# Kernel tuning notes

Hardware: AMD Instinct MI355X
Metric: run time of the kernel (lower is better)

Reference implementation:

```python
import jax, jax.numpy as jnp
import numpy as np

NEG = -1.0e4          # finite stand-in for log(0) to keep grads nan-free
DEN_SCALE = 1.0
B, T, P = 32, 500, 2048
S_DEN, S_NUM = 1024, 128


def setup_inputs() -> dict:
    key = jax.random.key(0)
    k0, k1 = jax.random.split(key)
    x = jax.random.normal(k0, (B, T, P), dtype=jnp.float32)
    seqlengths = jax.random.randint(k1, (B,), T // 2, T + 1)

    rng = np.random.default_rng(0)
    # --- denominator FSM (shared phone-LM lattice): self-loop + banded + random arcs ---
    idx = np.arange(S_DEN)
    mask = np.zeros((S_DEN, S_DEN), bool)
    for off in (0, 1, 2, 5):
        mask[idx, (idx + off) % S_DEN] = True
    mask[idx, rng.integers(0, S_DEN, S_DEN)] = True  # long-range arcs
    logw = rng.normal(0.0, 0.5, (S_DEN, S_DEN)).astype(np.float32)
    den_logT = jnp.asarray(np.where(mask, logw, NEG).astype(np.float32))
    den_init = jnp.full((S_DEN,), -np.log(S_DEN), dtype=jnp.float32)
    den_final = jnp.zeros((S_DEN,), dtype=jnp.float32)
    den_pdfmap = jnp.asarray(rng.integers(0, P, S_DEN))

    # --- numerator FSMs (per-utterance left-to-right alignment graphs) ---
    j = np.arange(S_NUM)
    nmask = np.zeros((S_NUM, S_NUM), bool)
    nmask[j, j] = True               # self-loops
    nmask[j[:-1], j[:-1] + 1] = True  # forward arcs
    nlogw = rng.normal(0.0, 0.5, (B, S_NUM, S_NUM)).astype(np.float32)
    num_logT = jnp.asarray(np.where(nmask[None], nlogw, NEG).astype(np.float32))
    num_init = jnp.asarray(np.where(j == 0, 0.0, NEG).astype(np.float32))
    nf = np.full(S_NUM, NEG, np.float32); nf[-1] = 0.0
    num_final = jnp.asarray(nf)
    num_pdfmap = jnp.asarray(rng.integers(0, P, (B, S_NUM)))

    return {
        'input': x, 'seqlengths': seqlengths,
        'den_logT': den_logT, 'den_init': den_init, 'den_final': den_final,
        'den_pdfmap': den_pdfmap,
        'num_logT': num_logT, 'num_init': num_init, 'num_final': num_final,
        'num_pdfmap': num_pdfmap,
    }


def _fsm_logmarginal(emis, seqlengths, logT, init, final):
    """Forward (alpha) recursion; returns per-utterance log-marginal [B].

    emis: [B,T,S] state emission log-likelihoods (already pdf-mapped)
    logT: [S,S] shared or [B,S,S] per-utterance log transition weights
    """
    Tmat = jnp.exp(logT)  # NEG -> ~0, recovers the sparse arc structure
    Bx, Tlen, S = emis.shape
    alpha = jnp.broadcast_to(init, (Bx, S)) + emis[:, 0]  # [B,S]

    def step(alpha, xt):
        e_t, t = xt
        # numerically stable log-matmul: logsumexp_i(alpha_i + logT_ij)
        m = jnp.max(alpha, axis=1, keepdims=True)            # [B,1]
        p = jnp.exp(alpha - m)                               # [B,S]
        if Tmat.ndim == 2:
            s = p @ Tmat                                     # [B,S]
        else:
            s = jnp.einsum('bi,bij->bj', p, Tmat)
        new = e_t + m + jnp.log(jnp.maximum(s, 1e-30))
        return jnp.where(t < seqlengths[:, None], new, alpha), None

    xs = (jnp.swapaxes(emis[:, 1:], 0, 1), jnp.arange(1, Tlen))
    alpha, _ = jax.lax.scan(step, alpha, xs)
    return jax.nn.logsumexp(alpha + final, axis=1)  # [B]


def reference(input, seqlengths, den_logT, den_init, den_final, den_pdfmap,
              num_logT, num_init, num_final, num_pdfmap):
    # map state -> pdf emission scores
    num_emis = jnp.take_along_axis(input, num_pdfmap[:, None, :], axis=2)  # [B,T,S_NUM]
    den_emis = input[:, :, den_pdfmap]                                      # [B,T,S_DEN]
    num_llh = jnp.sum(_fsm_logmarginal(num_emis, seqlengths, num_logT, num_init, num_final))
    den_llh = jnp.sum(_fsm_logmarginal(den_emis, seqlengths, den_logT, den_init, den_final))
    return -(num_llh - DEN_SCALE * den_llh)
```

## Files before the change

kernel.cpp:

```cpp
#include <hip/hip_runtime.h>

namespace {

constexpr int B = 32, T = 500, P = 2048;
constexpr int SD = 1024, SN = 128;
constexpr float NZ_THRESH = -5000.0f;
constexpr int MAXE = 12;

#define BAR_LDS() asm volatile("s_waitcnt lgkmcnt(0)\n\ts_barrier" ::: "memory")

template<int CTRL>
__device__ __forceinline__ float dpp_mov(float v, float old) {
  return __builtin_bit_cast(float, __builtin_amdgcn_update_dpp(
      __builtin_bit_cast(int, old), __builtin_bit_cast(int, v),
      CTRL, 0xf, 0xf, false));
}

__device__ __forceinline__ float wave_max_bcast(float v) {
  v = fmaxf(v, dpp_mov<0x111>(v, v));
  v = fmaxf(v, dpp_mov<0x112>(v, v));
  v = fmaxf(v, dpp_mov<0x114>(v, v));
  v = fmaxf(v, dpp_mov<0x118>(v, v));
  v = fmaxf(v, dpp_mov<0x142>(v, v));
  v = fmaxf(v, dpp_mov<0x143>(v, v));
  return __builtin_bit_cast(float,
      __builtin_amdgcn_readlane(__builtin_bit_cast(int, v), 63));
}

__device__ __forceinline__ float wave_sum_bcast(float v) {
  v += dpp_mov<0x111>(v, 0.0f);
  v += dpp_mov<0x112>(v, 0.0f);
  v += dpp_mov<0x114>(v, 0.0f);
  v += dpp_mov<0x118>(v, 0.0f);
  v += dpp_mov<0x142>(v, 0.0f);
  v += dpp_mov<0x143>(v, 0.0f);
  return __builtin_bit_cast(float,
      __builtin_amdgcn_readlane(__builtin_bit_cast(int, v), 63));
}

__device__ __forceinline__ float max4(float a, float b, float c, float d) {
  return fmaxf(fmaxf(a, b), fmaxf(c, d));
}


__global__ void k_init(int* __restrict__ rcount, float* __restrict__ out) {
  int i = blockIdx.x * blockDim.x + threadIdx.x;
  if (i < SD) rcount[i] = 0;
  if (i == 0) out[0] = 0.0f;
}

__device__ __forceinline__ bool is_det(int i, int j) {
  int off = (j - i) & (SD - 1);
  return off == 0 || off == 1 || off == 2 || off == 5;
}

__global__ void k_count(const float* __restrict__ dlogT, int* __restrict__ rcount) {
  int idx = blockIdx.x * blockDim.x + threadIdx.x;
  if (idx >= SD * SD) return;
  int i = idx >> 10, j = idx & (SD - 1);
  float v = dlogT[idx];
  if (v > NZ_THRESH && !is_det(i, j)) atomicAdd(&rcount[j], 1);
}

__global__ __launch_bounds__(1024) void k_scan(const int* __restrict__ rcount,
                                               int* __restrict__ rptr,
                                               int* __restrict__ wpos) {
  __shared__ int sA[SD], sB[SD];
  int tid = threadIdx.x;
  int v = rcount[tid];
  sA[tid] = v;
  __syncthreads();
  int* src = sA; int* dst = sB;
  for (int off = 1; off < SD; off <<= 1) {
    int val = src[tid];
    if (tid >= off) val += src[tid - off];
    dst[tid] = val;
    __syncthreads();
    int* t = src; src = dst; dst = t;
  }
  int inc = src[tid];
  rptr[tid + 1] = inc;
  if (tid == 0) rptr[0] = 0;
  wpos[tid] = inc - v;
}

__global__ void k_fill(const float* __restrict__ dlogT, int* __restrict__ wpos,
                       int2* __restrict__ compact) {
  int idx = blockIdx.x * blockDim.x + threadIdx.x;
  if (idx >= SD * SD) return;
  int i = idx >> 10, j = idx & (SD - 1);
  float v = dlogT[idx];
  if (v > NZ_THRESH && !is_det(i, j)) {
    int pos = atomicAdd(&wpos[j], 1);
    if (pos < 1024) compact[pos] = make_int2(i, __float_as_int(__expf(v)));
  }
}


__global__ __launch_bounds__(256) void lfmmi_main(
    const float* __restrict__ x, const int* __restrict__ seqlen,
    const float* __restrict__ dlogT, const float* __restrict__ dinit,
    const float* __restrict__ dfinal, const int* __restrict__ dpdf,
    const float* __restrict__ nlogT, const float* __restrict__ ninit,
    const float* __restrict__ nfinal, const int* __restrict__ npdf,
    const int* __restrict__ rptr, const int2* __restrict__ redge,
    float* __restrict__ out) {
  int bid = blockIdx.x;
  int tid = threadIdx.x;

  if (bid < B) {
    __shared__ __align__(16) float lp[SD + 8];
    __shared__ __align__(16) float wred[4];
    __shared__ int2 sedge[1024];

    const int b = bid;
    int L = seqlen[b]; if (L > T) L = T; if (L < 1) L = 1;
    const int s0 = tid * 4;
    const float* xb = x + (long)b * T * P;

    int nnz = rptr[SD]; if (nnz > 1024) nnz = 1024;
    for (int k = tid; k < nnz; k += 256) sedge[k] = redge[k];

    float dw[4][4];
    const int offs[4] = {0, 1, 2, 5};
#pragma unroll
    for (int i = 0; i < 4; ++i) {
      int j = s0 + i;
#pragma unroll
      for (int o = 0; o < 4; ++o) {
        int r = (j - offs[o]) & (SD - 1);
        dw[i][o] = __expf(dlogT[r * SD + j]);
      }
    }

    const int pdf0 = dpdf[s0], pdf1 = dpdf[s0 + 1], pdf2 = dpdf[s0 + 2], pdf3 = dpdf[s0 + 3];
    const int r0 = rptr[s0], r1 = rptr[s0 + 1], r2 = rptr[s0 + 2],
              r3 = rptr[s0 + 3], r4 = rptr[s0 + 4];

    int   erow[MAXE];
    float ew0[MAXE], ew1[MAXE], ew2[MAXE], ew3[MAXE];
#pragma unroll
    for (int s = 0; s < MAXE; ++s) {
      int k = r0 + s;
      bool valid = k < r4;
      int kk = valid ? k : 0;
      int2 e = redge[kk];
      erow[s] = valid ? e.x : 0;
      float w = __int_as_float(e.y);
      ew0[s] = (valid && k <  r1) ? w : 0.0f;
      ew1[s] = (valid && k >= r1 && k < r2) ? w : 0.0f;
      ew2[s] = (valid && k >= r2 && k < r3) ? w : 0.0f;
      ew3[s] = (valid && k >= r3) ? w : 0.0f;
    }
    const bool overflow = (r4 - r0) > MAXE;

    float4 al;
    al.x = dinit[s0]     + xb[pdf0];
    al.y = dinit[s0 + 1] + xb[pdf1];
    al.z = dinit[s0 + 2] + xb[pdf2];
    al.w = dinit[s0 + 3] + xb[pdf3];

    float4 ec, en, ef;
    ec.x = xb[P + pdf0];     ec.y = xb[P + pdf1];     ec.z = xb[P + pdf2];     ec.w = xb[P + pdf3];
    en.x = xb[2 * P + pdf0]; en.y = xb[2 * P + pdf1]; en.z = xb[2 * P + pdf2]; en.w = xb[2 * P + pdf3];

    __syncthreads();

    for (int t = 1; t < L; ++t) {
      float mw = wave_max_bcast(max4(al.x, al.y, al.z, al.w));
      if ((tid & 63) == 0) wred[tid >> 6] = mw;
      BAR_LDS();
      float4 wv = *(const float4*)wred;
      float m = max4(wv.x, wv.y, wv.z, wv.w);

      float4 p;
      p.x = expf(al.x - m); p.y = expf(al.y - m);
      p.z = expf(al.z - m); p.w = expf(al.w - m);
      *(float4*)&lp[8 + s0] = p;
      if (tid >= 254) *(float4*)&lp[8 + s0 - SD] = p;

      {
        int tp = t + 2; if (tp > T - 1) tp = T - 1;
        const float* xr = xb + tp * P;
        ef.x = xr[pdf0]; ef.y = xr[pdf1]; ef.z = xr[pdf2]; ef.w = xr[pdf3];
      }
      BAR_LDS();

      float4 w = *(const float4*)&lp[8 + s0 - 4];
      float pm5 = lp[8 + s0 - 5];
      float acc0 = p.x * dw[0][0] + w.w * dw[0][1] + w.z * dw[0][2] + pm5 * dw[0][3];
      float acc1 = p.y * dw[1][0] + p.x * dw[1][1] + w.w * dw[1][2] + w.x * dw[1][3];
      float acc2 = p.z * dw[2][0] + p.y * dw[2][1] + p.x * dw[2][2] + w.y * dw[2][3];
      float acc3 = p.w * dw[3][0] + p.z * dw[3][1] + p.y * dw[3][2] + w.z * dw[3][3];

#pragma unroll
      for (int s = 0; s < MAXE; ++s) {
        float val = lp[8 + erow[s]];
        acc0 += val * ew0[s];
        acc1 += val * ew1[s];
        acc2 += val * ew2[s];
        acc3 += val * ew3[s];
      }
      if (overflow) {
        for (int k = r0 + MAXE; k < r4; ++k) {
          int2 e = sedge[k];
          float val = lp[8 + e.x] * __int_as_float(e.y);
          if (k < r1) acc0 += val; else if (k < r2) acc1 += val;
          else if (k < r3) acc2 += val; else acc3 += val;
        }
      }

      al.x = ec.x + m + logf(fmaxf(acc0, 1e-30f));
      al.y = ec.y + m + logf(fmaxf(acc1, 1e-30f));
      al.z = ec.z + m + logf(fmaxf(acc2, 1e-30f));
      al.w = ec.w + m + logf(fmaxf(acc3, 1e-30f));
      ec = en; en = ef;
    }

    float4 v;
    v.x = al.x + dfinal[s0];     v.y = al.y + dfinal[s0 + 1];
    v.z = al.z + dfinal[s0 + 2]; v.w = al.w + dfinal[s0 + 3];
    float mw = wave_max_bcast(max4(v.x, v.y, v.z, v.w));
    if ((tid & 63) == 0) wred[tid >> 6] = mw;
    __syncthreads();
    float4 wv = *(const float4*)wred;
    float M = max4(wv.x, wv.y, wv.z, wv.w);
    float ls = expf(v.x - M) + expf(v.y - M) + expf(v.z - M) + expf(v.w - M);
    float sw = wave_sum_bcast(ls);
    __syncthreads();
    if ((tid & 63) == 0) wred[tid >> 6] = sw;
    __syncthreads();
    if (tid == 0) {
      float S = wred[0] + wred[1] + wred[2] + wred[3];
      atomicAdd(out, M + logf(S));
    }
  } else {
    if (tid >= 64) return;
    const int b = bid - B;
    int L = seqlen[b]; if (L > T) L = T; if (L < 1) L = 1;
    const int u = tid;
    const int j0 = 2 * u, j1 = 2 * u + 1;
    const float* nT = nlogT + (long)b * SN * SN;
    const float d0  = __expf(nT[j0 * SN + j0]);
    const float d1  = __expf(nT[j1 * SN + j1]);
    const float up0 = (j0 > 0) ? __expf(nT[(j0 - 1) * SN + j0]) : 0.0f;
    const float up1 = __expf(nT[j0 * SN + j1]);
    const int pdf0 = npdf[b * SN + j0], pdf1 = npdf[b * SN + j1];
    const float* xb = x + (long)b * T * P;

    float a0 = ninit[j0] + xb[pdf0];
    float a1 = ninit[j1] + xb[pdf1];
    float e0c = xb[P + pdf0],     e1c = xb[P + pdf1];
    float e0n = xb[2 * P + pdf0], e1n = xb[2 * P + pdf1];

    for (int t = 1; t < L; ++t) {
      float m = wave_max_bcast(fmaxf(a0, a1));
      float p0 = expf(a0 - m), p1 = expf(a1 - m);
      float pm = __shfl_up(p1, 1);
      int tp = t + 2; if (tp > T - 1) tp = T - 1;
      const float* xr = xb + tp * P;
      float e0f = xr[pdf0], e1f = xr[pdf1];
      float s0v = p0 * d0 + pm * up0;
      float s1v = p1 * d1 + p0 * up1;
      a0 = e0c + m + logf(fmaxf(s0v, 1e-30f));
      a1 = e1c + m + logf(fmaxf(s1v, 1e-30f));
      e0c = e0n; e1c = e1n; e0n = e0f; e1n = e1f;
    }

    float v0 = a0 + nfinal[j0], v1 = a1 + nfinal[j1];
    float M = wave_max_bcast(fmaxf(v0, v1));
    float S = wave_sum_bcast(expf(v0 - M) + expf(v1 - M));
    if (u == 0) atomicAdd(out, -(M + logf(S)));
  }
}

}

extern "C" void kernel_launch(void* const* d_in, const int* in_sizes, int n_in,
                              void* d_out, int out_size, void* d_ws, size_t ws_size,
                              hipStream_t stream) {
  const float* x      = (const float*)d_in[0];
  const int*   seqlen = (const int*)d_in[1];
  const float* dlogT  = (const float*)d_in[2];
  const float* dinit  = (const float*)d_in[3];
  const float* dfinal = (const float*)d_in[4];
  const int*   dpdf   = (const int*)d_in[5];
  const float* nlogT  = (const float*)d_in[6];
  const float* ninit  = (const float*)d_in[7];
  const float* nfinal = (const float*)d_in[8];
  const int*   npdf   = (const int*)d_in[9];
  float* out = (float*)d_out;

  char* ws = (char*)d_ws;
  int*  rcount  = (int*)(ws + 0);
  int*  rptr    = (int*)(ws + 8192);
  int*  wpos    = (int*)(ws + 16384);
  int2* compact = (int2*)(ws + 20480);

  hipLaunchKernelGGL(k_init,  dim3(4),    dim3(256),  0, stream, rcount, out);
  hipLaunchKernelGGL(k_count, dim3(4096), dim3(256),  0, stream, dlogT, rcount);
  hipLaunchKernelGGL(k_scan,  dim3(1),    dim3(1024), 0, stream, rcount, rptr, wpos);
  hipLaunchKernelGGL(k_fill,  dim3(4096), dim3(256),  0, stream, dlogT, wpos, compact);
  hipLaunchKernelGGL(lfmmi_main, dim3(2 * B), dim3(256), 0, stream,
                     x, seqlen, dlogT, dinit, dfinal, dpdf,
                     nlogT, ninit, nfinal, npdf, rptr, compact, out);
}
```

Measured before the change: 625.5 us.

## Double-buffer LDS state and defer block max to remove one barrier per step

Double-buffers the probability array and the per-wave max scratch in shared memory. Each step's block-wide max reduction is written at the end of the previous step and read after the single remaining barrier. This removes one workgroup barrier from each serial time step of the denominator forward recursion. The stabilising max used in the exponent is now taken from an earlier step rather than the current one. That is mathematically neutral but relies on alpha not drifting far enough in one step to overflow or underflow the exp.

```diff
diff --git a/kernel.cpp b/kernel.cpp
--- a/kernel.cpp
+++ b/kernel.cpp
@@ -109,8 +109,8 @@
   int tid = threadIdx.x;
 
   if (bid < B) {
-    __shared__ __align__(16) float lp[SD + 8];
-    __shared__ __align__(16) float wred[4];
+    __shared__ __align__(16) float lp[2][SD + 8];
+    __shared__ __align__(16) float wredb[2][4];
     __shared__ int2 sedge[1024];
 
     const int b = bid;
@@ -164,30 +164,36 @@
     ec.x = xb[P + pdf0];     ec.y = xb[P + pdf1];     ec.z = xb[P + pdf2];     ec.w = xb[P + pdf3];
     en.x = xb[2 * P + pdf0]; en.y = xb[2 * P + pdf1]; en.z = xb[2 * P + pdf2]; en.w = xb[2 * P + pdf3];
 
-    __syncthreads();
+    {
+      float mw = wave_max_bcast(max4(al.x, al.y, al.z, al.w));
+      if ((tid & 63) == 0) wredb[0][tid >> 6] = mw;
+    }
+    __syncthreads();
+    float m = max4(wredb[0][0], wredb[0][1], wredb[0][2], wredb[0][3]);
 
     for (int t = 1; t < L; ++t) {
-      float mw = wave_max_bcast(max4(al.x, al.y, al.z, al.w));
-      if ((tid & 63) == 0) wred[tid >> 6] = mw;
-      BAR_LDS();
-      float4 wv = *(const float4*)wred;
-      float m = max4(wv.x, wv.y, wv.z, wv.w);
+      const int cur = t & 1;
+      float* lpc = lp[cur];
 
       float4 p;
       p.x = expf(al.x - m); p.y = expf(al.y - m);
       p.z = expf(al.z - m); p.w = expf(al.w - m);
-      *(float4*)&lp[8 + s0] = p;
-      if (tid >= 254) *(float4*)&lp[8 + s0 - SD] = p;
+      *(float4*)&lpc[8 + s0] = p;
+      if (tid >= 254) *(float4*)&lpc[8 + s0 - SD] = p;
 
       {
         int tp = t + 2; if (tp > T - 1) tp = T - 1;
         const float* xr = xb + tp * P;
         ef.x = xr[pdf0]; ef.y = xr[pdf1]; ef.z = xr[pdf2]; ef.w = xr[pdf3];
       }
+
       BAR_LDS();
 
-      float4 w = *(const float4*)&lp[8 + s0 - 4];
-      float pm5 = lp[8 + s0 - 5];
+      float4 wv = *(const float4*)wredb[cur ^ 1];
+      float m_next = max4(wv.x, wv.y, wv.z, wv.w);
+
+      float4 w = *(const float4*)&lpc[8 + s0 - 4];
+      float pm5 = lpc[8 + s0 - 5];
       float acc0 = p.x * dw[0][0] + w.w * dw[0][1] + w.z * dw[0][2] + pm5 * dw[0][3];
       float acc1 = p.y * dw[1][0] + p.x * dw[1][1] + w.w * dw[1][2] + w.x * dw[1][3];
       float acc2 = p.z * dw[2][0] + p.y * dw[2][1] + p.x * dw[2][2] + w.y * dw[2][3];
@@ -195,7 +201,7 @@
 
 #pragma unroll
       for (int s = 0; s < MAXE; ++s) {
-        float val = lp[8 + erow[s]];
+        float val = lpc[8 + erow[s]];
         acc0 += val * ew0[s];
         acc1 += val * ew1[s];
         acc2 += val * ew2[s];
@@ -204,7 +210,7 @@
       if (overflow) {
         for (int k = r0 + MAXE; k < r4; ++k) {
           int2 e = sedge[k];
-          float val = lp[8 + e.x] * __int_as_float(e.y);
+          float val = lpc[8 + e.x] * __int_as_float(e.y);
           if (k < r1) acc0 += val; else if (k < r2) acc1 += val;
           else if (k < r3) acc2 += val; else acc3 += val;
         }
@@ -215,23 +221,29 @@
       al.z = ec.z + m + logf(fmaxf(acc2, 1e-30f));
       al.w = ec.w + m + logf(fmaxf(acc3, 1e-30f));
       ec = en; en = ef;
-    }
-
+
+      float mw = wave_max_bcast(max4(al.x, al.y, al.z, al.w));
+      if ((tid & 63) == 0) wredb[cur][tid >> 6] = mw;
+
+      m = m_next;
+    }
+
+    __syncthreads();
     float4 v;
     v.x = al.x + dfinal[s0];     v.y = al.y + dfinal[s0 + 1];
     v.z = al.z + dfinal[s0 + 2]; v.w = al.w + dfinal[s0 + 3];
     float mw = wave_max_bcast(max4(v.x, v.y, v.z, v.w));
-    if ((tid & 63) == 0) wred[tid >> 6] = mw;
-    __syncthreads();
-    float4 wv = *(const float4*)wred;
+    if ((tid & 63) == 0) wredb[0][tid >> 6] = mw;
+    __syncthreads();
+    float4 wv = *(const float4*)wredb[0];
     float M = max4(wv.x, wv.y, wv.z, wv.w);
     float ls = expf(v.x - M) + expf(v.y - M) + expf(v.z - M) + expf(v.w - M);
     float sw = wave_sum_bcast(ls);
     __syncthreads();
-    if ((tid & 63) == 0) wred[tid >> 6] = sw;
+    if ((tid & 63) == 0) wredb[0][tid >> 6] = sw;
     __syncthreads();
     if (tid == 0) {
-      float S = wred[0] + wred[1] + wred[2] + wred[3];
+      float S = wredb[0][0] + wredb[0][1] + wredb[0][2] + wredb[0][3];
       atomicAdd(out, M + logf(S));
     }
   } else {
```

New measurement: 557.3 us. -10.9%, faster.
